# Kernel optimization log

Hardware: AMD Instinct MI355X
Metric: run time of the kernel (lower is better)

## Reference

```python
import jax, jax.numpy as jnp
import numpy as np

N = 100000      # nodes
E = 800000      # edges
F_IN = 128      # input feature dim
HID = 32        # GAT out_channels per head
H = 4           # heads
HC = HID * H    # 128, concat width (== F_IN by design)
EDIM = 16       # raw edge feature dim
G = 256         # number of graphs in batch
OUT = 2         # output classes
SLOPE = 0.2     # GATConv LeakyReLU negative slope
BN_EPS = 1e-5


def setup_inputs() -> dict:
    key = jax.random.key(0)
    ks = jax.random.split(key, 16)
    s = 0.05
    x = jax.random.normal(ks[0], (N, F_IN), jnp.float32)
    edge_index = jax.random.randint(ks[1], (2, E), 0, N, dtype=jnp.int64)
    edge_attr = jax.random.normal(ks[2], (E, EDIM), jnp.float32)
    batch = jnp.sort(jax.random.randint(ks[3], (N,), 0, G, dtype=jnp.int64))
    edge_fc_W = jax.random.normal(ks[4], (EDIM, HID), jnp.float32) * s
    edge_fc_b = jnp.zeros((HID,), jnp.float32)
    # all 3 GAT layers have in_dim 128 -> H*C 128, so stack them
    Ws = jax.random.normal(ks[5], (3, F_IN, HC), jnp.float32) * s
    att_src = jax.random.normal(ks[6], (3, H, HID), jnp.float32) * s
    att_dst = jax.random.normal(ks[7], (3, H, HID), jnp.float32) * s
    att_edge = jax.random.normal(ks[8], (3, H, HID), jnp.float32) * s
    lin_e = jax.random.normal(ks[9], (3, HID, HC), jnp.float32) * s
    biases = jnp.zeros((3, HC), jnp.float32)
    bn_gamma = jnp.ones((3, HC), jnp.float32)
    bn_beta = jnp.zeros((3, HC), jnp.float32)
    fc_W = jax.random.normal(ks[10], (HC, OUT), jnp.float32) * s
    fc_b = jnp.zeros((OUT,), jnp.float32)
    return {"x": x, "edge_index": edge_index, "edge_attr": edge_attr, "batch": batch,
            "edge_fc_W": edge_fc_W, "edge_fc_b": edge_fc_b, "Ws": Ws,
            "att_src": att_src, "att_dst": att_dst, "att_edge": att_edge,
            "lin_e": lin_e, "biases": biases, "bn_gamma": bn_gamma,
            "bn_beta": bn_beta, "fc_W": fc_W, "fc_b": fc_b}


def _gat_layer(h, e_h, src, dst, W, a_s, a_d, a_e, We, b):
    xl = (h @ W).reshape(N, H, HID)            # [N,H,C]
    el = (e_h @ We).reshape(E, H, HID)         # [E,H,C]
    alpha = ((xl * a_s).sum(-1)[src]           # alpha_src gathered at source
             + (xl * a_d).sum(-1)[dst]         # alpha_dst gathered at target
             + (el * a_e).sum(-1))             # [E,H]
    alpha = jax.nn.leaky_relu(alpha, SLOPE)
    # segment softmax over incoming edges of each destination node
    amax = jax.ops.segment_max(alpha, dst, num_segments=N)
    ealpha = jnp.exp(alpha - amax[dst])
    denom = jax.ops.segment_sum(ealpha, dst, num_segments=N)
    alpha = ealpha / (denom[dst] + 1e-16)
    # weighted scatter-aggregate of source messages
    out = jax.ops.segment_sum(alpha[:, :, None] * xl[src], dst, num_segments=N)
    return out.reshape(N, HC) + b


def reference(x, edge_index, edge_attr, batch, edge_fc_W, edge_fc_b, Ws,
              att_src, att_dst, att_edge, lin_e, biases, bn_gamma, bn_beta,
              fc_W, fc_b):
    src, dst = edge_index[0], edge_index[1]
    e_h = edge_attr @ edge_fc_W + edge_fc_b   # [E, HID]
    h = x
    for l in range(3):
        h = _gat_layer(h, e_h, src, dst, Ws[l], att_src[l], att_dst[l],
                       att_edge[l], lin_e[l], biases[l])
        # BatchNorm1d over node dim (training-mode batch statistics)
        mu = h.mean(0)
        var = h.var(0)
        h = (h - mu) * jax.lax.rsqrt(var + BN_EPS) * bn_gamma[l] + bn_beta[l]
        h = jax.nn.relu(h)
        # dropout_rate = 0.0 -> identity
    # global mean pool per graph
    sums = jax.ops.segment_sum(h, batch, num_segments=G)
    cnt = jax.ops.segment_sum(jnp.ones((N,), h.dtype), batch, num_segments=G)
    pooled = sums / jnp.maximum(cnt, 1.0)[:, None]   # [G, HC]
    return pooled @ fc_W + fc_b                      # [G, OUT]
```

## Files before the change

kernel.cpp:

```cpp
#include <hip/hip_runtime.h>

#define Nn 100000
#define Ee 800000
#define HC 128
#define HID 32
#define NHD 4
#define EDIM 16
#define Gg 256
#define NOUT 2
#define SLOPE 0.2f
#define BN_EPS 1e-5f
#define SCHUNK 1024
#define NSB 98
#define NBAG 6250

typedef unsigned int u32;
typedef unsigned short u16;
typedef short v8s __attribute__((ext_vector_type(8)));
typedef float v4f __attribute__((ext_vector_type(4)));

union PkAB { u32 u[4]; v8s v; };

__device__ __forceinline__ float bflo(u32 u){ return __uint_as_float(u << 16); }
__device__ __forceinline__ float bfhi(u32 u){ return __uint_as_float(u & 0xFFFF0000u); }

__device__ __forceinline__ u32 bf16rne(float x)
{
  u32 b = __float_as_uint(x);
  return (b + 0x7FFFu + ((b >> 16) & 1u)) >> 16;
}
__device__ __forceinline__ u32 packsplit(float x)
{
  u32 hb = bf16rne(x);
  float hf = __uint_as_float(hb << 16);
  u32 lb = bf16rne(x - hf);
  return hb | (lb << 16);
}
__device__ __forceinline__ void split2(float f, u32& hb, u32& lb)
{
  hb = bf16rne(f);
  lb = bf16rne(f - __uint_as_float(hb << 16));
}

__global__ void compute_K(const float* __restrict__ efcW, const float* __restrict__ efcb,
                          const float* __restrict__ linE, const float* __restrict__ attE,
                          float* __restrict__ Kmat, float* __restrict__ kb)
{
  __shared__ float Msh[384];
  int t = threadIdx.x;
  if (t < 384) {
    int l = t >> 7, j = (t >> 2) & 31, h = t & 3;
    float m = 0.f;
    for (int c = 0; c < 32; ++c)
      m += linE[(l*32 + j)*128 + h*32 + c] * attE[(l*4 + h)*32 + c];
    Msh[l*128 + j*4 + h] = m;
  }
  __syncthreads();
  if (t < 192) {
    int k = t / 12, col = t % 12, l = col >> 2, h = col & 3;
    float acc = 0.f;
    for (int j = 0; j < 32; ++j)
      acc += efcW[k*32 + j] * Msh[l*128 + j*4 + h];
    Kmat[k*12 + col] = acc;
  } else if (t < 204) {
    int col = t - 192, l = col >> 2, h = col & 3;
    float acc = 0.f;
    for (int j = 0; j < 32; ++j)
      acc += efcb[j] * Msh[l*128 + j*4 + h];
    kb[col] = acc;
  }
}

__global__ void w_split(const float* __restrict__ Wall, u32* __restrict__ Wf)
{
  int tid = blockIdx.x * 256 + threadIdx.x;
  if (tid >= 3*HC*HC) return;
  int l = tid / (HC*HC);
  int rem = tid - l*HC*HC;
  int k = rem >> 7, n = rem & 127;
  u32 p = packsplit(Wall[tid]);
  int nt = n >> 4, col = n & 15;
  int ks = k >> 5, kin = k & 31, q = kin >> 3, j = kin & 7;
  int half = j >> 2, j4 = j & 3;
  int idx = ((((l*8 + nt)*4 + ks)*2 + half)*64 + q*16 + col)*4 + j4;
  Wf[idx] = p;
}

__global__ void k_hist(const int* __restrict__ dst, int* __restrict__ deg)
{
  int e = blockIdx.x * 256 + threadIdx.x;
  if (e < Ee) atomicAdd(&deg[dst[e]], 1);
}

__global__ void k_bsum(const int* __restrict__ deg, int* __restrict__ bsum)
{
  __shared__ int sh[256];
  int b = blockIdx.x, t = threadIdx.x;
  int s = 0;
  for (int i = t; i < SCHUNK; i += 256) {
    int idx = b*SCHUNK + i;
    if (idx < Nn) s += deg[idx];
  }
  sh[t] = s; __syncthreads();
  for (int o = 128; o; o >>= 1) { if (t < o) sh[t] += sh[t+o]; __syncthreads(); }
  if (!t) bsum[b] = sh[0];
}

__global__ void k_mid(const int* __restrict__ bsum, int* __restrict__ bpre, int* __restrict__ rowp)
{
  __shared__ int sh[NSB];
  int t = threadIdx.x;
  if (t < NSB) sh[t] = bsum[t];
  __syncthreads();
  if (!t) {
    int run = 0;
    for (int i = 0; i < NSB; ++i) { int v = sh[i]; sh[i] = run; run += v; }
    rowp[Nn] = run;
  }
  __syncthreads();
  if (t < NSB) bpre[t] = sh[t];
}

__global__ void k_scan(const int* __restrict__ deg, const int* __restrict__ bpre, int* __restrict__ rowp)
{
  __shared__ int sh[SCHUNK];
  int b = blockIdx.x, t = threadIdx.x;
  for (int i = t; i < SCHUNK; i += 256) {
    int idx = b*SCHUNK + i;
    sh[i] = (idx < Nn) ? deg[idx] : 0;
  }
  __syncthreads();
  if (!t) {
    int run = 0;
    for (int i = 0; i < SCHUNK; ++i) { int v = sh[i]; sh[i] = run; run += v; }
  }
  __syncthreads();
  int base = bpre[b];
  for (int i = t; i < SCHUNK; i += 256) {
    int idx = b*SCHUNK + i;
    if (idx < Nn) rowp[idx] = sh[i] + base;
  }
}

__global__ void k_fillpre(const int* __restrict__ src, const int* __restrict__ dst,
                          const float* __restrict__ eattr,
                          const float* __restrict__ Kmat, const float* __restrict__ kb,
                          const int* __restrict__ rowp, int* __restrict__ fill,
                          u32* __restrict__ rec)
{
  int e = blockIdx.x * 256 + threadIdx.x;
  if (e >= Ee) return;
  const float4* p = (const float4*)(eattr + (size_t)e * EDIM);
  float ea[16];
  #pragma unroll
  for (int qq = 0; qq < 4; ++qq) {
    float4 v = p[qq];
    ea[qq*4+0] = v.x; ea[qq*4+1] = v.y; ea[qq*4+2] = v.z; ea[qq*4+3] = v.w;
  }
  float ep[12];
  #pragma unroll
  for (int col = 0; col < 12; ++col) ep[col] = kb[col];
  #pragma unroll
  for (int k = 0; k < 16; ++k) {
    float v = ea[k];
    #pragma unroll
    for (int col = 0; col < 12; ++col) ep[col] += v * Kmat[k*12 + col];
  }
  int d = dst[e];
  int pos = rowp[d] + atomicAdd(&fill[d], 1);
  uint4 r0, r1;
  r0.x = bf16rne(ep[0])  | (bf16rne(ep[1])  << 16);
  r0.y = bf16rne(ep[2])  | (bf16rne(ep[3])  << 16);
  r0.z = bf16rne(ep[4])  | (bf16rne(ep[5])  << 16);
  r0.w = bf16rne(ep[6])  | (bf16rne(ep[7])  << 16);
  r1.x = bf16rne(ep[8])  | (bf16rne(ep[9])  << 16);
  r1.y = bf16rne(ep[10]) | (bf16rne(ep[11]) << 16);
  r1.z = (u32)src[e];
  r1.w = 0;
  uint4* rp = (uint4*)(rec + (size_t)pos * 8);
  rp[0] = r0; rp[1] = r1;
}

__device__ __forceinline__ int lbound(const int* __restrict__ a, int n, int key)
{
  int lo = 0, hi = n;
  while (lo < hi) {
    int mid = (lo + hi) >> 1;
    if (a[mid] < key) lo = mid + 1; else hi = mid;
  }
  return lo;
}

__global__ void k_gb(const int* __restrict__ batch, int* __restrict__ gb)
{
  int g = blockIdx.x * 256 + threadIdx.x;
  if (g <= Gg) gb[g] = lbound(batch, Nn, g);
}

__global__ void split_x(const float* __restrict__ src, u32* __restrict__ dst)
{
  int idx = blockIdx.x * 256 + threadIdx.x;
  if (idx >= Nn*HC/4) return;
  float4 v = ((const float4*)src)[idx];
  uint4 o;
  o.x = packsplit(v.x); o.y = packsplit(v.y);
  o.z = packsplit(v.z); o.w = packsplit(v.w);
  ((uint4*)dst)[idx] = o;
}

__global__ __launch_bounds__(256, 4) void gemm_mfma(const u32* __restrict__ Apk,
                                                    const u32* __restrict__ Wf,
                                                    u16* __restrict__ C2,
                                                    const float* __restrict__ aS,
                                                    const float* __restrict__ aD,
                                                    float* __restrict__ as_,
                                                    float* __restrict__ ad_,
                                                    const float* __restrict__ scb,
                                                    const float* __restrict__ shb,
                                                    int apply_bn)
{
  int t = threadIdx.x;
  int w = t >> 6, lane = t & 63;
  int col = lane & 15, q = lane >> 4;
  int rbase = blockIdx.x * 64 + w * 16;

  v4f acc[8];
  #pragma unroll
  for (int nt = 0; nt < 8; ++nt) acc[nt] = (v4f){0.f, 0.f, 0.f, 0.f};

  const uint4* Wf4 = (const uint4*)Wf;

  int ar = rbase + col;
  if (ar >= Nn) ar = Nn - 1;
  const uint4* pa = (const uint4*)(Apk + (size_t)ar*HC);
  uint4 ra[8];
  #pragma unroll
  for (int ks = 0; ks < 4; ++ks) {
    ra[2*ks]   = pa[ks*8 + q*2];
    ra[2*ks+1] = pa[ks*8 + q*2 + 1];
  }

  #pragma unroll
  for (int ks = 0; ks < 4; ++ks) {
    PkAB Ah, Al;
    int cb = ks*32 + q*8;
    uint4 r0 = ra[2*ks], r1 = ra[2*ks+1];
    if (!apply_bn) {
      Ah.u[0] = (r0.x & 0xFFFFu) | (r0.y << 16);
      Al.u[0] = (r0.x >> 16)     | (r0.y & 0xFFFF0000u);
      Ah.u[1] = (r0.z & 0xFFFFu) | (r0.w << 16);
      Al.u[1] = (r0.z >> 16)     | (r0.w & 0xFFFF0000u);
      Ah.u[2] = (r1.x & 0xFFFFu) | (r1.y << 16);
      Al.u[2] = (r1.x >> 16)     | (r1.y & 0xFFFF0000u);
      Ah.u[3] = (r1.z & 0xFFFFu) | (r1.w << 16);
      Al.u[3] = (r1.z >> 16)     | (r1.w & 0xFFFF0000u);
    } else {
      float4 sc0 = *(const float4*)(scb + cb), sc1 = *(const float4*)(scb + cb + 4);
      float4 sh0 = *(const float4*)(shb + cb), sh1 = *(const float4*)(shb + cb + 4);
      float f0 = fmaxf((bflo(r0.x)+bfhi(r0.x))*sc0.x + sh0.x, 0.f);
      float f1 = fmaxf((bflo(r0.y)+bfhi(r0.y))*sc0.y + sh0.y, 0.f);
      float f2 = fmaxf((bflo(r0.z)+bfhi(r0.z))*sc0.z + sh0.z, 0.f);
      float f3 = fmaxf((bflo(r0.w)+bfhi(r0.w))*sc0.w + sh0.w, 0.f);
      float f4 = fmaxf((bflo(r1.x)+bfhi(r1.x))*sc1.x + sh1.x, 0.f);
      float f5 = fmaxf((bflo(r1.y)+bfhi(r1.y))*sc1.y + sh1.y, 0.f);
      float f6 = fmaxf((bflo(r1.z)+bfhi(r1.z))*sc1.z + sh1.z, 0.f);
      float f7 = fmaxf((bflo(r1.w)+bfhi(r1.w))*sc1.w + sh1.w, 0.f);
      u32 hb0,lb0,hb1,lb1,hb2,lb2,hb3,lb3,hb4,lb4,hb5,lb5,hb6,lb6,hb7,lb7;
      split2(f0,hb0,lb0); split2(f1,hb1,lb1); split2(f2,hb2,lb2); split2(f3,hb3,lb3);
      split2(f4,hb4,lb4); split2(f5,hb5,lb5); split2(f6,hb6,lb6); split2(f7,hb7,lb7);
      Ah.u[0] = hb0 | (hb1 << 16);  Al.u[0] = lb0 | (lb1 << 16);
      Ah.u[1] = hb2 | (hb3 << 16);  Al.u[1] = lb2 | (lb3 << 16);
      Ah.u[2] = hb4 | (hb5 << 16);  Al.u[2] = lb4 | (lb5 << 16);
      Ah.u[3] = hb6 | (hb7 << 16);  Al.u[3] = lb6 | (lb7 << 16);
    }
    #pragma unroll
    for (int nt = 0; nt < 8; ++nt) {
      uint4 b0 = Wf4[((nt*4 + ks)*2 + 0)*64 + lane];
      uint4 b1 = Wf4[((nt*4 + ks)*2 + 1)*64 + lane];
      PkAB Bh, Bl;
      Bh.u[0] = (b0.x & 0xFFFFu) | (b0.y << 16);
      Bl.u[0] = (b0.x >> 16)     | (b0.y & 0xFFFF0000u);
      Bh.u[1] = (b0.z & 0xFFFFu) | (b0.w << 16);
      Bl.u[1] = (b0.z >> 16)     | (b0.w & 0xFFFF0000u);
      Bh.u[2] = (b1.x & 0xFFFFu) | (b1.y << 16);
      Bl.u[2] = (b1.x >> 16)     | (b1.y & 0xFFFF0000u);
      Bh.u[3] = (b1.z & 0xFFFFu) | (b1.w << 16);
      Bl.u[3] = (b1.z >> 16)     | (b1.w & 0xFFFF0000u);
      acc[nt] = __builtin_amdgcn_mfma_f32_16x16x32_bf16(Ah.v, Bh.v, acc[nt], 0, 0, 0);
      acc[nt] = __builtin_amdgcn_mfma_f32_16x16x32_bf16(Ah.v, Bl.v, acc[nt], 0, 0, 0);
      acc[nt] = __builtin_amdgcn_mfma_f32_16x16x32_bf16(Al.v, Bh.v, acc[nt], 0, 0, 0);
    }
  }

  #pragma unroll
  for (int reg = 0; reg < 4; ++reg) {
    int row = rbase + q*4 + reg;
    if (row < Nn) {
      #pragma unroll
      for (int nt = 0; nt < 8; ++nt)
        C2[(size_t)row*HC + nt*16 + col] = (u16)bf16rne(acc[nt][reg]);
    }
  }

  #pragma unroll
  for (int h = 0; h < 4; ++h) {
    float a0 = aS[32*h + col], a1 = aS[32*h + 16 + col];
    float d0 = aD[32*h + col], d1 = aD[32*h + 16 + col];
    #pragma unroll
    for (int reg = 0; reg < 4; ++reg) {
      float s1 = acc[2*h][reg]*a0 + acc[2*h+1][reg]*a1;
      float s2 = acc[2*h][reg]*d0 + acc[2*h+1][reg]*d1;
      s1 += __shfl_xor(s1, 1); s1 += __shfl_xor(s1, 2);
      s1 += __shfl_xor(s1, 4); s1 += __shfl_xor(s1, 8);
      s2 += __shfl_xor(s2, 1); s2 += __shfl_xor(s2, 2);
      s2 += __shfl_xor(s2, 4); s2 += __shfl_xor(s2, 8);
      if (col == 0) {
        int row = rbase + q*4 + reg;
        if (row < Nn) {
          as_[row*NHD + h] = s1;
          ad_[row*NHD + h] = s2;
        }
      }
    }
  }
}

__global__ __launch_bounds__(256) void aggregate(const int* __restrict__ rowp, const u32* __restrict__ rec,
                                                 const float* __restrict__ as_, const float* __restrict__ ad_,
                                                 int l, const u32* __restrict__ xl2,
                                                 const float* __restrict__ bias, u32* __restrict__ outp,
                                                 float* __restrict__ psum, float* __restrict__ psq)
{
  __shared__ float4 rsA[256], rsB[256], rqA[256], rqB[256];
  int t = threadIdx.x;
  int n = blockIdx.x * 16 + (t >> 4);
  int c8 = t & 15;
  int h = c8 >> 2;
  float o[8];
  #pragma unroll
  for (int k = 0; k < 8; ++k) o[k] = 0.f;
  if (n < Nn) {
    int idx = l*4 + h;
    int p = idx >> 1, sel = idx & 1;
    float adh = ad_[n*NHD + h];
    int beg = rowp[n], end = rowp[n+1];
    float acc[8];
    #pragma unroll
    for (int k = 0; k < 8; ++k) acc[k] = 0.f;
    float wsum = 0.f;
    int i = beg;
    for (; i + 8 <= end; i += 8) {
      u32 eu[8]; int s[8]; float av[8]; uint4 v[8];
      #pragma unroll
      for (int j = 0; j < 8; ++j) eu[j] = rec[(size_t)(i+j)*8 + p];
      #pragma unroll
      for (int j = 0; j < 8; ++j) s[j] = (int)rec[(size_t)(i+j)*8 + 6];
      #pragma unroll
      for (int j = 0; j < 8; ++j) av[j] = as_[s[j]*NHD + h];
      #pragma unroll
      for (int j = 0; j < 8; ++j) v[j] = *(const uint4*)(xl2 + (size_t)s[j] * 64 + c8*4);
      #pragma unroll
      for (int j = 0; j < 8; ++j) {
        float ep = sel ? bfhi(eu[j]) : bflo(eu[j]);
        float a = ep + av[j] + adh;
        a = (a > 0.f) ? a : SLOPE * a;
        float wj = __expf(a);
        acc[0] += wj*bflo(v[j].x); acc[1] += wj*bfhi(v[j].x);
        acc[2] += wj*bflo(v[j].y); acc[3] += wj*bfhi(v[j].y);
        acc[4] += wj*bflo(v[j].z); acc[5] += wj*bfhi(v[j].z);
        acc[6] += wj*bflo(v[j].w); acc[7] += wj*bfhi(v[j].w);
        wsum += wj;
      }
    }
    for (; i < end; ++i) {
      u32 eu = rec[(size_t)i*8 + p];
      int s = (int)rec[(size_t)i*8 + 6];
      float ep = sel ? bfhi(eu) : bflo(eu);
      float a = ep + as_[s*NHD + h] + adh;
      a = (a > 0.f) ? a : SLOPE * a;
      float wj = __expf(a);
      uint4 v = *(const uint4*)(xl2 + (size_t)s * 64 + c8*4);
      acc[0] += wj*bflo(v.x); acc[1] += wj*bfhi(v.x);
      acc[2] += wj*bflo(v.y); acc[3] += wj*bfhi(v.y);
      acc[4] += wj*bflo(v.z); acc[5] += wj*bfhi(v.z);
      acc[6] += wj*bflo(v.w); acc[7] += wj*bfhi(v.w);
      wsum += wj;
    }
    float inv = 1.f / (wsum + 1e-16f);
    uint4 w0, w1;
    #pragma unroll
    for (int k = 0; k < 8; ++k) o[k] = acc[k]*inv + bias[c8*8 + k];
    w0.x = packsplit(o[0]); w0.y = packsplit(o[1]);
    w0.z = packsplit(o[2]); w0.w = packsplit(o[3]);
    w1.x = packsplit(o[4]); w1.y = packsplit(o[5]);
    w1.z = packsplit(o[6]); w1.w = packsplit(o[7]);
    uint4* op = (uint4*)(outp + (size_t)n * HC + c8*8);
    op[0] = w0; op[1] = w1;
  }
  rsA[t] = make_float4(o[0], o[1], o[2], o[3]);
  rsB[t] = make_float4(o[4], o[5], o[6], o[7]);
  rqA[t] = make_float4(o[0]*o[0], o[1]*o[1], o[2]*o[2], o[3]*o[3]);
  rqB[t] = make_float4(o[4]*o[4], o[5]*o[5], o[6]*o[6], o[7]*o[7]);
  __syncthreads();
  for (int off = 128; off >= 16; off >>= 1) {
    if (t < off) {
      rsA[t].x += rsA[t+off].x; rsA[t].y += rsA[t+off].y;
      rsA[t].z += rsA[t+off].z; rsA[t].w += rsA[t+off].w;
      rsB[t].x += rsB[t+off].x; rsB[t].y += rsB[t+off].y;
      rsB[t].z += rsB[t+off].z; rsB[t].w += rsB[t+off].w;
      rqA[t].x += rqA[t+off].x; rqA[t].y += rqA[t+off].y;
      rqA[t].z += rqA[t+off].z; rqA[t].w += rqA[t+off].w;
      rqB[t].x += rqB[t+off].x; rqB[t].y += rqB[t+off].y;
      rqB[t].z += rqB[t+off].z; rqB[t].w += rqB[t+off].w;
    }
    __syncthreads();
  }
  if (t < 16) {
    float4* ps = (float4*)(psum + (size_t)blockIdx.x*HC + t*8);
    ps[0] = rsA[t]; ps[1] = rsB[t];
    float4* pq = (float4*)(psq + (size_t)blockIdx.x*HC + t*8);
    pq[0] = rqA[t]; pq[1] = rqB[t];
  }
}

__global__ __launch_bounds__(256) void k_bnpart(const float* __restrict__ psum, const float* __restrict__ psq,
                                                float* __restrict__ gsum, float* __restrict__ gsq)
{
  __shared__ float4 rs[256], rq[256];
  int t = threadIdx.x;
  int c4 = t & 31, rg = t >> 5;
  float4 s = make_float4(0.f,0.f,0.f,0.f), q = make_float4(0.f,0.f,0.f,0.f);
  for (int k = blockIdx.x*8 + rg; k < NBAG; k += 64*8) {
    float4 a = *(const float4*)(psum + (size_t)k*HC + c4*4);
    float4 b = *(const float4*)(psq  + (size_t)k*HC + c4*4);
    s.x += a.x; s.y += a.y; s.z += a.z; s.w += a.w;
    q.x += b.x; q.y += b.y; q.z += b.z; q.w += b.w;
  }
  rs[t] = s; rq[t] = q;
  __syncthreads();
  for (int off = 128; off >= 32; off >>= 1) {
    if (t < off) {
      rs[t].x += rs[t+off].x; rs[t].y += rs[t+off].y;
      rs[t].z += rs[t+off].z; rs[t].w += rs[t+off].w;
      rq[t].x += rq[t+off].x; rq[t].y += rq[t+off].y;
      rq[t].z += rq[t+off].z; rq[t].w += rq[t+off].w;
    }
    __syncthreads();
  }
  if (t < 32) {
    atomicAdd(&gsum[t*4+0], rs[t].x); atomicAdd(&gsum[t*4+1], rs[t].y);
    atomicAdd(&gsum[t*4+2], rs[t].z); atomicAdd(&gsum[t*4+3], rs[t].w);
    atomicAdd(&gsq[t*4+0], rq[t].x);  atomicAdd(&gsq[t*4+1], rq[t].y);
    atomicAdd(&gsq[t*4+2], rq[t].z);  atomicAdd(&gsq[t*4+3], rq[t].w);
  }
}

__global__ void k_bnfin(float* __restrict__ gsum, float* __restrict__ gsq,
                        const float* __restrict__ gammaL, const float* __restrict__ betaL,
                        float* __restrict__ scb, float* __restrict__ shb)
{
  int c = threadIdx.x;
  float s = gsum[c], q = gsq[c];
  float mu  = s * (1.f / Nn);
  float var = q * (1.f / Nn) - mu * mu;
  float sc = rsqrtf(var + BN_EPS) * gammaL[c];
  scb[c] = sc;
  shb[c] = betaL[c] - mu * sc;
  gsum[c] = 0.f; gsq[c] = 0.f;
}

__global__ __launch_bounds__(256) void pool2(const u32* __restrict__ Ap, const int* __restrict__ gb,
                                             const float* __restrict__ scb, const float* __restrict__ shb,
                                             float* __restrict__ pool)
{
  __shared__ float4 red[256];
  int g = blockIdx.x >> 2, qt = blockIdx.x & 3;
  int t = threadIdx.x;
  int cg = t & 7;
  int rs = t >> 3;
  int c4 = qt*8 + cg;
  int c = c4 * 4;
  int lo = gb[g], hi = gb[g+1];
  float4 s4 = *(const float4*)(scb + c);
  float4 t4 = *(const float4*)(shb + c);
  float4 acc = make_float4(0.f,0.f,0.f,0.f);
  for (int n = lo + rs; n < hi; n += 32) {
    uint4 v = *(const uint4*)(Ap + (size_t)n*HC + c);
    acc.x += fmaxf((bflo(v.x)+bfhi(v.x))*s4.x + t4.x, 0.f);
    acc.y += fmaxf((bflo(v.y)+bfhi(v.y))*s4.y + t4.y, 0.f);
    acc.z += fmaxf((bflo(v.z)+bfhi(v.z))*s4.z + t4.z, 0.f);
    acc.w += fmaxf((bflo(v.w)+bfhi(v.w))*s4.w + t4.w, 0.f);
  }
  red[t] = acc;
  __syncthreads();
  for (int off = 128; off >= 8; off >>= 1) {
    if (t < off) {
      red[t].x += red[t+off].x; red[t].y += red[t+off].y;
      red[t].z += red[t+off].z; red[t].w += red[t+off].w;
    }
    __syncthreads();
  }
  if (t < 8) {
    float inv = 1.f / fmaxf((float)(hi - lo), 1.f);
    float4 r = red[t];
    r.x *= inv; r.y *= inv; r.z *= inv; r.w *= inv;
    *(float4*)(pool + (size_t)g*HC + qt*32 + t*4) = r;
  }
}

__global__ void final_fc(const float* __restrict__ pool,
                         const float* __restrict__ fcW, const float* __restrict__ fcb,
                         float* __restrict__ out)
{
  int t = blockIdx.x * 256 + threadIdx.x;
  if (t >= Gg * NOUT) return;
  int g = t >> 1, o = t & 1;
  float acc = 0.f;
  for (int k = 0; k < HC; ++k)
    acc += pool[(size_t)g * HC + k] * fcW[k * NOUT + o];
  out[t] = acc + fcb[o];
}

extern "C" void kernel_launch(void* const* d_in, const int* in_sizes, int n_in,
                              void* d_out, int out_size, void* d_ws, size_t ws_size,
                              hipStream_t stream)
{
  const float* x      = (const float*)d_in[0];
  const int*   eidx   = (const int*)d_in[1];
  const float* eattr  = (const float*)d_in[2];
  const int*   batch  = (const int*)d_in[3];
  const float* efcW   = (const float*)d_in[4];
  const float* efcb   = (const float*)d_in[5];
  const float* Wall   = (const float*)d_in[6];
  const float* attS   = (const float*)d_in[7];
  const float* attD   = (const float*)d_in[8];
  const float* attE   = (const float*)d_in[9];
  const float* linE   = (const float*)d_in[10];
  const float* biases = (const float*)d_in[11];
  const float* gamma  = (const float*)d_in[12];
  const float* beta   = (const float*)d_in[13];
  const float* fcW    = (const float*)d_in[14];
  const float* fcb    = (const float*)d_in[15];
  float* out = (float*)d_out;

  const int* src = eidx;
  const int* dst = eidx + Ee;

  float* ws    = (float*)d_ws;
  float* bufA  = ws;
  float* bufB  = bufA + (size_t)Nn*HC;
  float* as_   = bufB + (size_t)Nn*HC;
  float* ad_   = as_ + (size_t)Nn*NHD;
  float* Kmat  = ad_ + (size_t)Nn*NHD;
  float* kb    = Kmat + 192;
  float* scb   = kb + 16;
  float* shb   = scb + 128;
  float* gsum  = shb + 128;
  float* gsq   = gsum + 128;
  float* pool  = gsq + 128;
  u32*   rec   = (u32*)(pool + (size_t)Gg*HC);
  u32*   Wf    = rec + (size_t)Ee*8;
  float* psum  = (float*)(Wf + 3*HC*HC);
  float* psq   = psum + (size_t)NBAG*HC;
  int*   gb    = (int*)(psq + (size_t)NBAG*HC);
  int*   rowp  = gb + (Gg + 3);
  int*   deg   = rowp + (Nn + 1);
  int*   fill  = deg + Nn;
  int*   bsum  = fill + Nn;
  int*   bpre  = bsum + 128;

  w_split<<<(3*HC*HC + 255)/256, 256, 0, stream>>>(Wall, Wf);
  compute_K<<<1, 512, 0, stream>>>(efcW, efcb, linE, attE, Kmat, kb);
  k_gb<<<2, 256, 0, stream>>>(batch, gb);

  hipMemsetAsync(deg, 0, 2*Nn*sizeof(int), stream);
  hipMemsetAsync(gsum, 0, 256*sizeof(float), stream);
  k_hist<<<(Ee + 255)/256, 256, 0, stream>>>(dst, deg);
  k_bsum<<<NSB, 256, 0, stream>>>(deg, bsum);
  k_mid<<<1, 128, 0, stream>>>(bsum, bpre, rowp);
  k_scan<<<NSB, 256, 0, stream>>>(deg, bpre, rowp);
  k_fillpre<<<(Ee + 255)/256, 256, 0, stream>>>(src, dst, eattr, Kmat, kb, rowp, fill, rec);

  split_x<<<(Nn*HC/4 + 255)/256, 256, 0, stream>>>(x, (u32*)bufA);

  for (int l = 0; l < 3; ++l) {
    gemm_mfma<<<(Nn + 63)/64, 256, 0, stream>>>((const u32*)bufA, Wf + (size_t)l*HC*HC, (u16*)bufB,
                                                attS + l*HC, attD + l*HC, as_, ad_,
                                                scb, shb, (l > 0) ? 1 : 0);
    aggregate<<<NBAG, 256, 0, stream>>>(rowp, rec, as_, ad_, l, (const u32*)bufB,
                                        biases + l*HC, (u32*)bufA, psum, psq);
    k_bnpart<<<64, 256, 0, stream>>>(psum, psq, gsum, gsq);
    k_bnfin<<<1, 128, 0, stream>>>(gsum, gsq, gamma + l*HC, beta + l*HC, scb, shb);
  }

  pool2<<<Gg*4, 256, 0, stream>>>((const u32*)bufA, gb, scb, shb, pool);
  final_fc<<<2, 256, 0, stream>>>(pool, fcW, fcb, out);
}
```

Measured before the change: 647.8 us.

## Stage GEMM weight tiles in LDS and add 4-edge unrolled aggregation tail

In the MFMA GEMM, each k-step's weight fragments are now loaded cooperatively into shared memory by the whole block, and the four waves read from there instead of each fetching them from global memory. This adds two barriers per k-step and removes the full unroll of the ks loop. In the edge aggregation kernel, a 4-wide unrolled loop is added between the 8-wide main loop and the scalar tail, so more gathers are in flight for leftover edges. The aim is less redundant global/L2 traffic for weights and better latency hiding for low-degree nodes.

```diff
diff --git a/kernel.cpp b/kernel.cpp
--- a/kernel.cpp
+++ b/kernel.cpp
@@ -219,6 +219,7 @@
                                                     const float* __restrict__ shb,
                                                     int apply_bn)
 {
+  __shared__ uint4 Bsh[1024];
   int t = threadIdx.x;
   int w = t >> 6, lane = t & 63;
   int col = lane & 15, q = lane >> 4;
@@ -240,8 +241,15 @@
     ra[2*ks+1] = pa[ks*8 + q*2 + 1];
   }
 
-  #pragma unroll
   for (int ks = 0; ks < 4; ++ks) {
+    #pragma unroll
+    for (int i = 0; i < 4; ++i) {
+      int u = t + i*256;
+      int nt = u >> 7, rem = u & 127;
+      Bsh[u] = Wf4[((nt*4 + ks)*2 + (rem >> 6))*64 + (rem & 63)];
+    }
+    __syncthreads();
+
     PkAB Ah, Al;
     int cb = ks*32 + q*8;
     uint4 r0 = ra[2*ks], r1 = ra[2*ks+1];
@@ -275,8 +283,8 @@
     }
     #pragma unroll
     for (int nt = 0; nt < 8; ++nt) {
-      uint4 b0 = Wf4[((nt*4 + ks)*2 + 0)*64 + lane];
-      uint4 b1 = Wf4[((nt*4 + ks)*2 + 1)*64 + lane];
+      uint4 b0 = Bsh[nt*128 + lane];
+      uint4 b1 = Bsh[nt*128 + 64 + lane];
       PkAB Bh, Bl;
       Bh.u[0] = (b0.x & 0xFFFFu) | (b0.y << 16);
       Bl.u[0] = (b0.x >> 16)     | (b0.y & 0xFFFF0000u);
@@ -290,6 +298,7 @@
       acc[nt] = __builtin_amdgcn_mfma_f32_16x16x32_bf16(Ah.v, Bl.v, acc[nt], 0, 0, 0);
       acc[nt] = __builtin_amdgcn_mfma_f32_16x16x32_bf16(Al.v, Bh.v, acc[nt], 0, 0, 0);
     }
+    __syncthreads();
   }
 
   #pragma unroll
@@ -361,6 +370,29 @@
       for (int j = 0; j < 8; ++j) v[j] = *(const uint4*)(xl2 + (size_t)s[j] * 64 + c8*4);
       #pragma unroll
       for (int j = 0; j < 8; ++j) {
+        float ep = sel ? bfhi(eu[j]) : bflo(eu[j]);
+        float a = ep + av[j] + adh;
+        a = (a > 0.f) ? a : SLOPE * a;
+        float wj = __expf(a);
+        acc[0] += wj*bflo(v[j].x); acc[1] += wj*bfhi(v[j].x);
+        acc[2] += wj*bflo(v[j].y); acc[3] += wj*bfhi(v[j].y);
+        acc[4] += wj*bflo(v[j].z); acc[5] += wj*bfhi(v[j].z);
+        acc[6] += wj*bflo(v[j].w); acc[7] += wj*bfhi(v[j].w);
+        wsum += wj;
+      }
+    }
+    for (; i + 4 <= end; i += 4) {
+      u32 eu[4]; int s[4]; float av[4]; uint4 v[4];
+      #pragma unroll
+      for (int j = 0; j < 4; ++j) eu[j] = rec[(size_t)(i+j)*8 + p];
+      #pragma unroll
+      for (int j = 0; j < 4; ++j) s[j] = (int)rec[(size_t)(i+j)*8 + 6];
+      #pragma unroll
+      for (int j = 0; j < 4; ++j) av[j] = as_[s[j]*NHD + h];
+      #pragma unroll
+      for (int j = 0; j < 4; ++j) v[j] = *(const uint4*)(xl2 + (size_t)s[j] * 64 + c8*4);
+      #pragma unroll
+      for (int j = 0; j < 4; ++j) {
         float ep = sel ? bfhi(eu[j]) : bflo(eu[j]);
         float a = ep + av[j] + adh;
         a = (a > 0.f) ? a : SLOPE * a;
```

After: 610.0 us. -5.8%, faster.
